# Optimization experiments

Measured on AMD Instinct MI355X. Metric: run time of the kernel, lower is better.

## Reference

```python
import jax, jax.numpy as jnp
import numpy as np

N_NODES = 50000
N_EDGES = 800000
IN_DIM = 128
HIDDEN = 128


def setup_inputs() -> dict:
    key = jax.random.key(0)
    ks = jax.random.split(key, 6)
    x = jax.random.normal(ks[0], (N_NODES, IN_DIM), dtype=jnp.float32)
    edge_index = jax.random.randint(ks[1], (2, N_EDGES), 0, N_NODES, dtype=jnp.int32)
    W1 = jax.random.normal(ks[2], (IN_DIM, HIDDEN), dtype=jnp.float32) * 0.05
    b1 = jnp.zeros((HIDDEN,), dtype=jnp.float32)
    W2 = jax.random.normal(ks[3], (HIDDEN, HIDDEN), dtype=jnp.float32) * 0.05
    b2 = jnp.zeros((HIDDEN,), dtype=jnp.float32)
    return {"x": x, "edge_index": edge_index, "W1": W1, "b1": b1, "W2": W2, "b2": b2}


def _gcn_conv(x, W, b, src, dst, norm, n):
    # PyG GCNConv: linear transform, then normalized sum-aggregate, then bias.
    h = x @ W                                  # [N, H]
    msg = h[src] * norm[:, None]               # gather + scale  [E+N, H]
    out = jax.ops.segment_sum(msg, dst, num_segments=n)
    return out + b


def reference(x, edge_index, W1, b1, W2, b2):
    n = x.shape[0]
    # add self-loops (GCNConv default add_self_loops=True)
    loops = jnp.arange(n, dtype=edge_index.dtype)
    src = jnp.concatenate([edge_index[0], loops])
    dst = jnp.concatenate([edge_index[1], loops])
    # symmetric normalization: deg over destination nodes (edge_weight = 1)
    deg = jax.ops.segment_sum(jnp.ones(src.shape, dtype=x.dtype), dst, num_segments=n)
    dinv = jax.lax.rsqrt(deg)                  # deg >= 1 because of self-loops
    norm = dinv[src] * dinv[dst]               # [E+N]
    h = jax.nn.relu(_gcn_conv(x, W1, b1, src, dst, norm, n))
    return _gcn_conv(h, W2, b2, src, dst, norm, n)
```

## Files before the change

### kernel.cpp

```cpp
#include <hip/hip_runtime.h>

#define N_NODES 50000
#define N_EDGES 800000
#define DIM 128
#define CHUNK 4096
#define GRID 196
#define SEG_CAP 6144
#define GEMM_BLOCKS 391
#define GA 196
#define GB (GEMM_BLOCKS - GA)

typedef __attribute__((ext_vector_type(8))) short bf16x8;
typedef __attribute__((ext_vector_type(4))) float f32x4;


__device__ inline unsigned rne_bf16(float f) {
    unsigned u = __float_as_uint(f);
    return (u + 0x7FFFu + ((u >> 16) & 1u)) >> 16;
}
__device__ inline unsigned pk_bf16(float a, float b) {
    return rne_bf16(a) | (rne_bf16(b) << 16);
}
__device__ inline float bf_lo(unsigned u) { return __uint_as_float(u << 16); }
__device__ inline float bf_hi(unsigned u) { return __uint_as_float(u & 0xFFFF0000u); }


__device__ void fragw_build(const float* __restrict__ W, uint4* __restrict__ fh,
                            uint4* __restrict__ fl, int slot) {
    const int lane = slot & 63, tile = slot >> 6;
    const int c = tile >> 2, q = tile & 3;
    const int k0 = q * 32 + ((lane >> 4) << 3);
    const int col = c * 16 + (lane & 15);
    unsigned h[8], l[8];
#pragma unroll
    for (int j = 0; j < 8; ++j) {
        float w = W[(size_t)(k0 + j) * DIM + col];
        unsigned hb = rne_bf16(w);
        h[j] = hb;
        l[j] = rne_bf16(w - __uint_as_float(hb << 16));
    }
    uint4 uh, ul;
    uh.x = h[0] | (h[1] << 16); uh.y = h[2] | (h[3] << 16);
    uh.z = h[4] | (h[5] << 16); uh.w = h[6] | (h[7] << 16);
    ul.x = l[0] | (l[1] << 16); ul.y = l[2] | (l[3] << 16);
    ul.z = l[4] | (l[5] << 16); ul.w = l[6] | (l[7] << 16);
    fh[slot] = uh;
    fl[slot] = ul;
}


__global__ __launch_bounds__(256) void chunk_hist_fragw(const int* __restrict__ dst,
                                                        int* __restrict__ chist,
                                                        const float* __restrict__ W1,
                                                        const float* __restrict__ W2,
                                                        uint4* f1h, uint4* f1l,
                                                        uint4* f2h, uint4* f2l) {
    const int bid = blockIdx.x;
    if (bid < GRID) {
        __shared__ int hist[256];
        const int t = threadIdx.x;
        const int eb = bid * CHUNK;
        const int cnt = min(CHUNK, N_EDGES - eb);
        hist[t] = 0;
        __syncthreads();
        for (int i = t; i < cnt; i += 256)
            atomicAdd(&hist[dst[eb + i] >> 8], 1);
        __syncthreads();
        chist[bid * 256 + t] = hist[t];
    } else {
        const int b2 = bid - GRID;
        const int slot = (b2 & 7) * 256 + threadIdx.x;
        if (b2 < 8) fragw_build(W1, f1h, f1l, slot);
        else        fragw_build(W2, f2h, f2l, slot);
    }
}


__device__ void gemm_body(const float* __restrict__ X,
                          const uint4* __restrict__ fWh,
                          const uint4* __restrict__ fWl,
                          uint2* __restrict__ O, int gb, char* smem) {
    const int t = threadIdx.x;

    {
        uint4* s4 = (uint4*)smem;
        for (int i = t; i < 2048; i += 256) {
            s4[i] = fWh[i];
            s4[2048 + i] = fWl[i];
        }
    }
    __syncthreads();

    const int w = t >> 6, lane = t & 63;
    const int lrow = lane & 15, lgrp = lane >> 4;
    const int rbase = gb * 128;

    bf16x8 Ah[2][4], Al[2][4];
#pragma unroll
    for (int m = 0; m < 2; ++m) {
        const int r = rbase + w * 32 + m * 16 + lrow;
        const bool ok = (r < N_NODES);
        const float4* xp = (const float4*)(X + (size_t)r * DIM + lgrp * 8);
#pragma unroll
        for (int q = 0; q < 4; ++q) {
            float4 a0 = ok ? xp[q * 8]     : make_float4(0.f, 0.f, 0.f, 0.f);
            float4 a1 = ok ? xp[q * 8 + 1] : make_float4(0.f, 0.f, 0.f, 0.f);
            float f[8] = {a0.x, a0.y, a0.z, a0.w, a1.x, a1.y, a1.z, a1.w};
            bf16x8 hi, lo;
#pragma unroll
            for (int j = 0; j < 8; ++j) {
                unsigned hb = rne_bf16(f[j]);
                hi[j] = (short)hb;
                lo[j] = (short)rne_bf16(f[j] - __uint_as_float(hb << 16));
            }
            Ah[m][q] = hi;
            Al[m][q] = lo;
        }
    }

    f32x4 acc[2][8];
#pragma unroll
    for (int m = 0; m < 2; ++m)
#pragma unroll
        for (int c = 0; c < 8; ++c)
            acc[m][c] = (f32x4){0.f, 0.f, 0.f, 0.f};

    const bf16x8* Bh = (const bf16x8*)smem;
    const bf16x8* Bl = (const bf16x8*)(smem + 32768);
#pragma unroll
    for (int c = 0; c < 8; ++c) {
#pragma unroll
        for (int q = 0; q < 4; ++q) {
            bf16x8 bh = Bh[(c * 4 + q) * 64 + lane];
            bf16x8 bl = Bl[(c * 4 + q) * 64 + lane];
#pragma unroll
            for (int m = 0; m < 2; ++m) {
                acc[m][c] = __builtin_amdgcn_mfma_f32_16x16x32_bf16(Ah[m][q], bh, acc[m][c], 0, 0, 0);
                acc[m][c] = __builtin_amdgcn_mfma_f32_16x16x32_bf16(Al[m][q], bh, acc[m][c], 0, 0, 0);
                acc[m][c] = __builtin_amdgcn_mfma_f32_16x16x32_bf16(Ah[m][q], bl, acc[m][c], 0, 0, 0);
            }
        }
    }

    __syncthreads();
    float* Lf = (float*)smem;
#pragma unroll
    for (int m = 0; m < 2; ++m)
#pragma unroll
        for (int c = 0; c < 8; ++c)
#pragma unroll
            for (int rg = 0; rg < 4; ++rg)
                Lf[(w * 32 + m * 16 + lgrp * 4 + rg) * DIM + c * 16 + lrow] = acc[m][c][rg];
    __syncthreads();

    const float4* Lf4 = (const float4*)smem;
    for (int idx = t; idx < 4096; idx += 256) {
        const int row = idx >> 5, s = idx & 31;
        const int gr = rbase + row;
        if (gr < N_NODES) {
            float4 v = Lf4[idx];
            uint2 o;
            o.x = pk_bf16(v.x, v.y);
            o.y = pk_bf16(v.z, v.w);
            O[(size_t)gr * 32 + s] = o;
        }
    }
}


__device__ void sort_scatter_body(const int* __restrict__ src,
                                  const int* __restrict__ dst,
                                  const int* __restrict__ chist,
                                  unsigned* __restrict__ sorted,
                                  int* __restrict__ bbase_g,
                                  int bid, char* smem) {
    int* hist  = (int*)smem;
    int* sc    = hist + 256;
    int* lbase = sc + 256;
    int* lcur  = lbase + 256;
    int* gbase = lcur + 256;
    unsigned* sl = (unsigned*)(smem + 5 * 1024);

    const int t = threadIdx.x;
    const int eb = bid * CHUNK;
    const int cnt = min(CHUNK, N_EDGES - eb);

    int sum = 0, myoff = 0;
    for (int c = 0; c < GRID; ++c) {
        int v = chist[c * 256 + t];
        if (c == bid) myoff = sum;
        sum += v;
    }
    hist[t] = chist[bid * 256 + t];
    sc[t] = sum;
    __syncthreads();
    for (int off = 1; off < 256; off <<= 1) {
        int u = (t >= off) ? sc[t - off] : 0;
        __syncthreads();
        sc[t] += u;
        __syncthreads();
    }
    gbase[t] = (sc[t] - sum) + myoff;
    if (bid == 0) bbase_g[t] = sc[t] - sum;
    __syncthreads();

    sc[t] = hist[t];
    __syncthreads();
    for (int off = 1; off < 256; off <<= 1) {
        int u = (t >= off) ? sc[t - off] : 0;
        __syncthreads();
        sc[t] += u;
        __syncthreads();
    }
    int ex = sc[t] - hist[t];
    lbase[t] = ex;
    lcur[t] = ex;
    __syncthreads();

    for (int i = t; i < cnt; i += 256) {
        int s = src[eb + i], d = dst[eb + i];
        int b = d >> 8;
        int p = atomicAdd(&lcur[b], 1);
        sl[p] = ((unsigned)b << 24) | ((unsigned)(d & 255) << 16) | (unsigned)s;
    }
    __syncthreads();
    for (int i = t; i < cnt; i += 256) {
        unsigned rec = sl[i];
        int b = rec >> 24;
        sorted[gbase[b] + (i - lbase[b])] = rec;
    }
}


__device__ void csr_build_body(const unsigned* __restrict__ sorted,
                               const int* __restrict__ bbase,
                               int* __restrict__ rowptr,
                               float* __restrict__ dinv,
                               int* __restrict__ csr,
                               int k, char* smem) {
    int* hist = (int*)smem;
    int* sc   = hist + 256;
    int* lcur = sc + 256;
    int* seg  = (int*)(smem + 3 * 1024);

    const int t = threadIdx.x;
    const int base = bbase[k];
    const int cntk = ((k == 255) ? N_EDGES : bbase[k + 1]) - base;
    if (k == 0 && t == 0) rowptr[N_NODES] = N_EDGES;

    hist[t] = 0;
    __syncthreads();
    for (int i = t; i < cntk; i += 256)
        atomicAdd(&hist[(sorted[base + i] >> 16) & 255], 1);
    __syncthreads();

    const int node = (k << 8) + t;
    const int dv = hist[t];
    if (node < N_NODES) dinv[node] = rsqrtf((float)dv + 1.0f);

    sc[t] = dv;
    __syncthreads();
    for (int off = 1; off < 256; off <<= 1) {
        int u = (t >= off) ? sc[t - off] : 0;
        __syncthreads();
        sc[t] += u;
        __syncthreads();
    }
    int ex = sc[t] - dv;
    if (node < N_NODES) rowptr[node] = base + ex;
    lcur[t] = ex;
    __syncthreads();

    if (cntk <= SEG_CAP) {
        for (int i = t; i < cntk; i += 256) {
            unsigned rec = sorted[base + i];
            int p = atomicAdd(&lcur[(rec >> 16) & 255], 1);
            seg[p] = (int)(rec & 0xFFFFu);
        }
        __syncthreads();
        for (int i = t; i < cntk; i += 256)
            csr[base + i] = seg[i];
    } else {
        for (int i = t; i < cntk; i += 256) {
            unsigned rec = sorted[base + i];
            int p = atomicAdd(&lcur[(rec >> 16) & 255], 1);
            csr[base + p] = (int)(rec & 0xFFFFu);
        }
    }
}


__global__ __launch_bounds__(256, 2) void sort_gemm(const int* __restrict__ src,
                                                    const int* __restrict__ dst,
                                                    const int* __restrict__ chist,
                                                    unsigned* __restrict__ sorted,
                                                    int* __restrict__ bbase_g,
                                                    const float* __restrict__ X,
                                                    const uint4* __restrict__ fWh,
                                                    const uint4* __restrict__ fWl,
                                                    uint2* __restrict__ O) {
    __shared__ __align__(16) char smem[65536];
    if (blockIdx.x < GRID)
        sort_scatter_body(src, dst, chist, sorted, bbase_g, blockIdx.x, smem);
    else
        gemm_body(X, fWh, fWl, O, blockIdx.x - GRID, smem);
}

__global__ __launch_bounds__(256, 2) void csr_gemm(const unsigned* __restrict__ sorted,
                                                   const int* __restrict__ bbase,
                                                   int* __restrict__ rowptr,
                                                   float* __restrict__ dinv,
                                                   int* __restrict__ csr,
                                                   const float* __restrict__ X,
                                                   const uint4* __restrict__ fWh,
                                                   const uint4* __restrict__ fWl,
                                                   uint2* __restrict__ O) {
    __shared__ __align__(16) char smem[65536];
    if (blockIdx.x < GRID)
        csr_build_body(sorted, bbase, rowptr, dinv, csr, blockIdx.x, smem);
    else
        gemm_body(X, fWh, fWl, O, blockIdx.x - GRID + GA, smem);
}


__device__ inline float4 agg_node(int node, const uint2* __restrict__ H2,
                                  const int* __restrict__ rowptr,
                                  const int* __restrict__ csr,
                                  const float* __restrict__ dinv,
                                  const float4* __restrict__ b4, int relu) {
    const int lane = threadIdx.x & 63;
    const int half = lane >> 5;
    const int col  = lane & 31;

    const float dn = dinv[node];
    float4 acc = make_float4(0.f, 0.f, 0.f, 0.f);
    if (half == 0) {
        uint2 v = H2[(size_t)node * 32 + col];
        acc.x = dn * bf_lo(v.x); acc.y = dn * bf_hi(v.x);
        acc.z = dn * bf_lo(v.y); acc.w = dn * bf_hi(v.y);
    }

    int j = rowptr[node];
    const int end = rowptr[node + 1];

#define ACC(v, ds) do { \
        acc.x = fmaf((ds), bf_lo((v).x), acc.x); \
        acc.y = fmaf((ds), bf_hi((v).x), acc.y); \
        acc.z = fmaf((ds), bf_lo((v).y), acc.z); \
        acc.w = fmaf((ds), bf_hi((v).y), acc.w); } while (0)

    for (; j + 16 <= end; j += 16) {
        int s0 = csr[j +  0 + half], s1 = csr[j +  2 + half];
        int s2 = csr[j +  4 + half], s3 = csr[j +  6 + half];
        int s4 = csr[j +  8 + half], s5 = csr[j + 10 + half];
        int s6 = csr[j + 12 + half], s7 = csr[j + 14 + half];
        uint2 v0 = H2[(size_t)s0 * 32 + col]; float d0 = dinv[s0];
        uint2 v1 = H2[(size_t)s1 * 32 + col]; float d1 = dinv[s1];
        uint2 v2 = H2[(size_t)s2 * 32 + col]; float d2 = dinv[s2];
        uint2 v3 = H2[(size_t)s3 * 32 + col]; float d3 = dinv[s3];
        uint2 v4 = H2[(size_t)s4 * 32 + col]; float d4 = dinv[s4];
        uint2 v5 = H2[(size_t)s5 * 32 + col]; float d5 = dinv[s5];
        uint2 v6 = H2[(size_t)s6 * 32 + col]; float d6 = dinv[s6];
        uint2 v7 = H2[(size_t)s7 * 32 + col]; float d7 = dinv[s7];
        ACC(v0, d0); ACC(v1, d1); ACC(v2, d2); ACC(v3, d3);
        ACC(v4, d4); ACC(v5, d5); ACC(v6, d6); ACC(v7, d7);
    }
    if (j + 8 <= end) {
        int s0 = csr[j + half], s1 = csr[j + 2 + half];
        int s2 = csr[j + 4 + half], s3 = csr[j + 6 + half];
        uint2 v0 = H2[(size_t)s0 * 32 + col]; float d0 = dinv[s0];
        uint2 v1 = H2[(size_t)s1 * 32 + col]; float d1 = dinv[s1];
        uint2 v2 = H2[(size_t)s2 * 32 + col]; float d2 = dinv[s2];
        uint2 v3 = H2[(size_t)s3 * 32 + col]; float d3 = dinv[s3];
        ACC(v0, d0); ACC(v1, d1); ACC(v2, d2); ACC(v3, d3);
        j += 8;
    }
    if (j + 4 <= end) {
        int s0 = csr[j + half], s1 = csr[j + 2 + half];
        uint2 v0 = H2[(size_t)s0 * 32 + col]; float d0 = dinv[s0];
        uint2 v1 = H2[(size_t)s1 * 32 + col]; float d1 = dinv[s1];
        ACC(v0, d0); ACC(v1, d1);
        j += 4;
    }
    if (j + 2 <= end) {
        int s = csr[j + half];
        uint2 v = H2[(size_t)s * 32 + col]; float d0 = dinv[s];
        ACC(v, d0);
        j += 2;
    }
    if (j < end && half == 0) {
        int s = csr[j];
        uint2 v = H2[(size_t)s * 32 + col]; float d0 = dinv[s];
        ACC(v, d0);
    }
#undef ACC

    acc.x += __shfl_xor(acc.x, 32, 64);
    acc.y += __shfl_xor(acc.y, 32, 64);
    acc.z += __shfl_xor(acc.z, 32, 64);
    acc.w += __shfl_xor(acc.w, 32, 64);

    float4 o = make_float4(0.f, 0.f, 0.f, 0.f);
    if (half == 0) {
        float4 bb = b4[col];
        o.x = acc.x * dn + bb.x;
        o.y = acc.y * dn + bb.y;
        o.z = acc.z * dn + bb.z;
        o.w = acc.w * dn + bb.w;
        if (relu) {
            o.x = fmaxf(o.x, 0.f); o.y = fmaxf(o.y, 0.f);
            o.z = fmaxf(o.z, 0.f); o.w = fmaxf(o.w, 0.f);
        }
    }
    return o;
}


__global__ __launch_bounds__(256) void aggregate_h1(const uint2* __restrict__ H2,
                                                    const int* __restrict__ rowptr,
                                                    const int* __restrict__ csr,
                                                    const float* __restrict__ dinv,
                                                    const float4* __restrict__ b4,
                                                    uint2* __restrict__ h1h,
                                                    uint2* __restrict__ h1l) {
    int node = blockIdx.x * 4 + (threadIdx.x >> 6);
    if (node >= N_NODES) return;
    float4 o = agg_node(node, H2, rowptr, csr, dinv, b4, 1);
    const int lane = threadIdx.x & 63;
    if (lane < 32) {
        unsigned hx = rne_bf16(o.x), hy = rne_bf16(o.y);
        unsigned hz = rne_bf16(o.z), hw = rne_bf16(o.w);
        unsigned lx = rne_bf16(o.x - __uint_as_float(hx << 16));
        unsigned ly = rne_bf16(o.y - __uint_as_float(hy << 16));
        unsigned lz = rne_bf16(o.z - __uint_as_float(hz << 16));
        unsigned lw = rne_bf16(o.w - __uint_as_float(hw << 16));
        uint2 hv; hv.x = hx | (hy << 16); hv.y = hz | (hw << 16);
        uint2 lv; lv.x = lx | (ly << 16); lv.y = lz | (lw << 16);
        h1h[(size_t)node * 32 + lane] = hv;
        h1l[(size_t)node * 32 + lane] = lv;
    }
}


__global__ __launch_bounds__(256) void aggregate_out(const uint2* __restrict__ H2,
                                                     const int* __restrict__ rowptr,
                                                     const int* __restrict__ csr,
                                                     const float* __restrict__ dinv,
                                                     const float4* __restrict__ b4,
                                                     float4* __restrict__ out) {
    int node = blockIdx.x * 4 + (threadIdx.x >> 6);
    if (node >= N_NODES) return;
    float4 o = agg_node(node, H2, rowptr, csr, dinv, b4, 0);
    const int lane = threadIdx.x & 63;
    if (lane < 32) out[(size_t)node * 32 + lane] = o;
}


__global__ __launch_bounds__(256, 2) void gemm_xw2(const uint2* __restrict__ h1h,
                                                   const uint2* __restrict__ h1l,
                                                   const uint4* __restrict__ fWh,
                                                   const uint4* __restrict__ fWl,
                                                   uint2* __restrict__ O) {
    __shared__ __align__(16) char smem[65536];
    const int t = threadIdx.x;

    {
        uint4* s4 = (uint4*)smem;
        for (int i = t; i < 2048; i += 256) {
            s4[i] = fWh[i];
            s4[2048 + i] = fWl[i];
        }
    }
    __syncthreads();

    const int w = t >> 6, lane = t & 63;
    const int lrow = lane & 15, lgrp = lane >> 4;
    const int rbase = blockIdx.x * 128;

    bf16x8 Ah[2][4], Al[2][4];
    const bf16x8 zz = (bf16x8){0,0,0,0,0,0,0,0};
#pragma unroll
    for (int m = 0; m < 2; ++m) {
        const int r = rbase + w * 32 + m * 16 + lrow;
        const bool ok = (r < N_NODES);
        const uint2* ph = h1h + (size_t)r * 32 + lgrp * 2;
        const uint2* pl = h1l + (size_t)r * 32 + lgrp * 2;
#pragma unroll
        for (int q = 0; q < 4; ++q) {
            Ah[m][q] = ok ? *(const bf16x8*)(ph + q * 8) : zz;
            Al[m][q] = ok ? *(const bf16x8*)(pl + q * 8) : zz;
        }
    }

    f32x4 acc[2][8];
#pragma unroll
    for (int m = 0; m < 2; ++m)
#pragma unroll
        for (int c = 0; c < 8; ++c)
            acc[m][c] = (f32x4){0.f, 0.f, 0.f, 0.f};

    const bf16x8* Bh = (const bf16x8*)smem;
    const bf16x8* Bl = (const bf16x8*)(smem + 32768);
#pragma unroll
    for (int c = 0; c < 8; ++c) {
#pragma unroll
        for (int q = 0; q < 4; ++q) {
            bf16x8 bh = Bh[(c * 4 + q) * 64 + lane];
            bf16x8 bl = Bl[(c * 4 + q) * 64 + lane];
#pragma unroll
            for (int m = 0; m < 2; ++m) {
                acc[m][c] = __builtin_amdgcn_mfma_f32_16x16x32_bf16(Ah[m][q], bh, acc[m][c], 0, 0, 0);
                acc[m][c] = __builtin_amdgcn_mfma_f32_16x16x32_bf16(Al[m][q], bh, acc[m][c], 0, 0, 0);
                acc[m][c] = __builtin_amdgcn_mfma_f32_16x16x32_bf16(Ah[m][q], bl, acc[m][c], 0, 0, 0);
            }
        }
    }

    __syncthreads();
    float* Lf = (float*)smem;
#pragma unroll
    for (int m = 0; m < 2; ++m)
#pragma unroll
        for (int c = 0; c < 8; ++c)
#pragma unroll
            for (int rg = 0; rg < 4; ++rg)
                Lf[(w * 32 + m * 16 + lgrp * 4 + rg) * DIM + c * 16 + lrow] = acc[m][c][rg];
    __syncthreads();

    const float4* Lf4 = (const float4*)smem;
    for (int idx = t; idx < 4096; idx += 256) {
        const int row = idx >> 5, s = idx & 31;
        const int gr = rbase + row;
        if (gr < N_NODES) {
            float4 v = Lf4[idx];
            uint2 o;
            o.x = pk_bf16(v.x, v.y);
            o.y = pk_bf16(v.z, v.w);
            O[(size_t)gr * 32 + s] = o;
        }
    }
}


extern "C" void kernel_launch(void* const* d_in, const int* in_sizes, int n_in,
                              void* d_out, int out_size, void* d_ws, size_t ws_size,
                              hipStream_t stream) {
    const float* x  = (const float*)d_in[0];
    const int*   ei = (const int*)d_in[1];
    const float* W1 = (const float*)d_in[2];
    const float* b1 = (const float*)d_in[3];
    const float* W2 = (const float*)d_in[4];
    const float* b2 = (const float*)d_in[5];
    float* out = (float*)d_out;

    const int* src = ei;
    const int* dst = ei + N_EDGES;

    char* p = (char*)d_ws;
    int*      chist  = (int*)p;              p += GRID * 256 * 4;
    float*    dinv   = (float*)p;            p += ((N_NODES * 4 + 1023) & ~1023);
    int*      rowptr = (int*)p;              p += (((N_NODES + 1) * 4 + 1023) & ~1023);
    unsigned* sorted = (unsigned*)p;         p += ((N_EDGES * 4 + 1023) & ~1023);
    int*      csr    = (int*)p;              p += ((N_EDGES * 4 + 1023) & ~1023);
    int*      bbase  = (int*)p;              p += 1024;
    uint4*    f1h    = (uint4*)p;            p += 32768;
    uint4*    f1l    = (uint4*)p;            p += 32768;
    uint4*    f2h    = (uint4*)p;            p += 32768;
    uint4*    f2l    = (uint4*)p;            p += 32768;
    uint2*    hp     = (uint2*)p;            p += (size_t)N_NODES * DIM * 2;
    uint2*    h1h    = (uint2*)p;            p += (size_t)N_NODES * DIM * 2;
    uint2*    h1l    = (uint2*)p;            p += (size_t)N_NODES * DIM * 2;
    uint2*    hp2    = (uint2*)p;

    const int aggBlocks = (N_NODES + 3) / 4;

    chunk_hist_fragw<<<GRID + 16, 256, 0, stream>>>(dst, chist, W1, W2,
                                                    f1h, f1l, f2h, f2l);
    sort_gemm<<<GRID + GA, 256, 0, stream>>>(src, dst, chist, sorted, bbase,
                                             x, f1h, f1l, hp);
    csr_gemm<<<GRID + GB, 256, 0, stream>>>(sorted, bbase, rowptr, dinv, csr,
                                            x, f1h, f1l, hp);

    aggregate_h1<<<aggBlocks, 256, 0, stream>>>(hp, rowptr, csr, dinv,
                                                (const float4*)b1, h1h, h1l);

    gemm_xw2<<<GEMM_BLOCKS, 256, 0, stream>>>(h1h, h1l, f2h, f2l, hp2);

    aggregate_out<<<aggBlocks, 256, 0, stream>>>(hp2, rowptr, csr, dinv,
                                                 (const float4*)b2, (float4*)out);
}
```

Before: 210.9 us.

## Prescale GEMM outputs by source dinv to drop per-edge dinv gathers

```diff
diff --git a/kernel.cpp b/kernel.cpp
--- a/kernel.cpp
+++ b/kernel.cpp
@@ -25,6 +25,12 @@
 __device__ inline float bf_hi(unsigned u) { return __uint_as_float(u & 0xFFFF0000u); }
 
 
+__global__ __launch_bounds__(256) void zero_deg(int* __restrict__ deg) {
+    const int i = blockIdx.x * 256 + threadIdx.x;
+    if (i < N_NODES) deg[i] = 0;
+}
+
+
 __device__ void fragw_build(const float* __restrict__ W, uint4* __restrict__ fh,
                             uint4* __restrict__ fl, int slot) {
     const int lane = slot & 63, tile = slot >> 6;
@@ -51,6 +57,7 @@
 
 __global__ __launch_bounds__(256) void chunk_hist_fragw(const int* __restrict__ dst,
                                                         int* __restrict__ chist,
+                                                        int* __restrict__ deg,
                                                         const float* __restrict__ W1,
                                                         const float* __restrict__ W2,
                                                         uint4* f1h, uint4* f1l,
@@ -63,8 +70,11 @@
         const int cnt = min(CHUNK, N_EDGES - eb);
         hist[t] = 0;
         __syncthreads();
-        for (int i = t; i < cnt; i += 256)
-            atomicAdd(&hist[dst[eb + i] >> 8], 1);
+        for (int i = t; i < cnt; i += 256) {
+            int d = dst[eb + i];
+            atomicAdd(&hist[d >> 8], 1);
+            atomicAdd(&deg[d], 1);
+        }
         __syncthreads();
         chist[bid * 256 + t] = hist[t];
     } else {
@@ -79,6 +89,7 @@
 __device__ void gemm_body(const float* __restrict__ X,
                           const uint4* __restrict__ fWh,
                           const uint4* __restrict__ fWl,
+                          const int* __restrict__ deg,
                           uint2* __restrict__ O, int gb, char* smem) {
     const int t = threadIdx.x;
 
@@ -158,10 +169,11 @@
         const int row = idx >> 5, s = idx & 31;
         const int gr = rbase + row;
         if (gr < N_NODES) {
+            float di = rsqrtf((float)deg[gr] + 1.0f);
             float4 v = Lf4[idx];
             uint2 o;
-            o.x = pk_bf16(v.x, v.y);
-            o.y = pk_bf16(v.z, v.w);
+            o.x = pk_bf16(v.x * di, v.y * di);
+            o.y = pk_bf16(v.z * di, v.w * di);
             O[(size_t)gr * 32 + s] = o;
         }
     }
@@ -298,12 +310,13 @@
                                                     const float* __restrict__ X,
                                                     const uint4* __restrict__ fWh,
                                                     const uint4* __restrict__ fWl,
+                                                    const int* __restrict__ deg,
                                                     uint2* __restrict__ O) {
     __shared__ __align__(16) char smem[65536];
     if (blockIdx.x < GRID)
         sort_scatter_body(src, dst, chist, sorted, bbase_g, blockIdx.x, smem);
     else
-        gemm_body(X, fWh, fWl, O, blockIdx.x - GRID, smem);
+        gemm_body(X, fWh, fWl, deg, O, blockIdx.x - GRID, smem);
 }
 
 __global__ __launch_bounds__(256, 2) void csr_gemm(const unsigned* __restrict__ sorted,
@@ -314,86 +327,84 @@
                                                    const float* __restrict__ X,
                                                    const uint4* __restrict__ fWh,
                                                    const uint4* __restrict__ fWl,
+                                                   const int* __restrict__ deg,
                                                    uint2* __restrict__ O) {
     __shared__ __align__(16) char smem[65536];
     if (blockIdx.x < GRID)
         csr_build_body(sorted, bbase, rowptr, dinv, csr, blockIdx.x, smem);
     else
-        gemm_body(X, fWh, fWl, O, blockIdx.x - GRID + GA, smem);
-}
-
-
-__device__ inline float4 agg_node(int node, const uint2* __restrict__ H2,
-                                  const int* __restrict__ rowptr,
-                                  const int* __restrict__ csr,
-                                  const float* __restrict__ dinv,
-                                  const float4* __restrict__ b4, int relu) {
+        gemm_body(X, fWh, fWl, deg, O, blockIdx.x - GRID + GA, smem);
+}
+
+
+__device__ inline float4 agg_node_ps(int node, const uint2* __restrict__ H2,
+                                     const int* __restrict__ rowptr,
+                                     const int* __restrict__ csr,
+                                     const float* __restrict__ dinv,
+                                     const float4* __restrict__ b4, int relu) {
     const int lane = threadIdx.x & 63;
     const int half = lane >> 5;
     const int col  = lane & 31;
 
-    const float dn = dinv[node];
     float4 acc = make_float4(0.f, 0.f, 0.f, 0.f);
     if (half == 0) {
         uint2 v = H2[(size_t)node * 32 + col];
-        acc.x = dn * bf_lo(v.x); acc.y = dn * bf_hi(v.x);
-        acc.z = dn * bf_lo(v.y); acc.w = dn * bf_hi(v.y);
+        acc.x = bf_lo(v.x); acc.y = bf_hi(v.x);
+        acc.z = bf_lo(v.y); acc.w = bf_hi(v.y);
     }
 
     int j = rowptr[node];
     const int end = rowptr[node + 1];
 
-#define ACC(v, ds) do { \
-        acc.x = fmaf((ds), bf_lo((v).x), acc.x); \
-        acc.y = fmaf((ds), bf_hi((v).x), acc.y); \
-        acc.z = fmaf((ds), bf_lo((v).y), acc.z); \
-        acc.w = fmaf((ds), bf_hi((v).y), acc.w); } while (0)
+#define ACCUM(v) do { \
+        acc.x += bf_lo((v).x); acc.y += bf_hi((v).x); \
+        acc.z += bf_lo((v).y); acc.w += bf_hi((v).y); } while (0)
 
     for (; j + 16 <= end; j += 16) {
         int s0 = csr[j +  0 + half], s1 = csr[j +  2 + half];
         int s2 = csr[j +  4 + half], s3 = csr[j +  6 + half];
         int s4 = csr[j +  8 + half], s5 = csr[j + 10 + half];
         int s6 = csr[j + 12 + half], s7 = csr[j + 14 + half];
-        uint2 v0 = H2[(size_t)s0 * 32 + col]; float d0 = dinv[s0];
-        uint2 v1 = H2[(size_t)s1 * 32 + col]; float d1 = dinv[s1];
-        uint2 v2 = H2[(size_t)s2 * 32 + col]; float d2 = dinv[s2];
-        uint2 v3 = H2[(size_t)s3 * 32 + col]; float d3 = dinv[s3];
-        uint2 v4 = H2[(size_t)s4 * 32 + col]; float d4 = dinv[s4];
-        uint2 v5 = H2[(size_t)s5 * 32 + col]; float d5 = dinv[s5];
-        uint2 v6 = H2[(size_t)s6 * 32 + col]; float d6 = dinv[s6];
-        uint2 v7 = H2[(size_t)s7 * 32 + col]; float d7 = dinv[s7];
-        ACC(v0, d0); ACC(v1, d1); ACC(v2, d2); ACC(v3, d3);
-        ACC(v4, d4); ACC(v5, d5); ACC(v6, d6); ACC(v7, d7);
+        uint2 v0 = H2[(size_t)s0 * 32 + col];
+        uint2 v1 = H2[(size_t)s1 * 32 + col];
+        uint2 v2 = H2[(size_t)s2 * 32 + col];
+        uint2 v3 = H2[(size_t)s3 * 32 + col];
+        uint2 v4 = H2[(size_t)s4 * 32 + col];
+        uint2 v5 = H2[(size_t)s5 * 32 + col];
+        uint2 v6 = H2[(size_t)s6 * 32 + col];
+        uint2 v7 = H2[(size_t)s7 * 32 + col];
+        ACCUM(v0); ACCUM(v1); ACCUM(v2); ACCUM(v3);
+        ACCUM(v4); ACCUM(v5); ACCUM(v6); ACCUM(v7);
     }
     if (j + 8 <= end) {
         int s0 = csr[j + half], s1 = csr[j + 2 + half];
         int s2 = csr[j + 4 + half], s3 = csr[j + 6 + half];
-        uint2 v0 = H2[(size_t)s0 * 32 + col]; float d0 = dinv[s0];
-        uint2 v1 = H2[(size_t)s1 * 32 + col]; float d1 = dinv[s1];
-        uint2 v2 = H2[(size_t)s2 * 32 + col]; float d2 = dinv[s2];
-        uint2 v3 = H2[(size_t)s3 * 32 + col]; float d3 = dinv[s3];
-        ACC(v0, d0); ACC(v1, d1); ACC(v2, d2); ACC(v3, d3);
+        uint2 v0 = H2[(size_t)s0 * 32 + col];
+        uint2 v1 = H2[(size_t)s1 * 32 + col];
+        uint2 v2 = H2[(size_t)s2 * 32 + col];
+        uint2 v3 = H2[(size_t)s3 * 32 + col];
+        ACCUM(v0); ACCUM(v1); ACCUM(v2); ACCUM(v3);
         j += 8;
     }
     if (j + 4 <= end) {
         int s0 = csr[j + half], s1 = csr[j + 2 + half];
-        uint2 v0 = H2[(size_t)s0 * 32 + col]; float d0 = dinv[s0];
-        uint2 v1 = H2[(size_t)s1 * 32 + col]; float d1 = dinv[s1];
-        ACC(v0, d0); ACC(v1, d1);
+        uint2 v0 = H2[(size_t)s0 * 32 + col];
+        uint2 v1 = H2[(size_t)s1 * 32 + col];
+        ACCUM(v0); ACCUM(v1);
         j += 4;
     }
     if (j + 2 <= end) {
         int s = csr[j + half];
-        uint2 v = H2[(size_t)s * 32 + col]; float d0 = dinv[s];
-        ACC(v, d0);
+        uint2 v = H2[(size_t)s * 32 + col];
+        ACCUM(v);
         j += 2;
     }
     if (j < end && half == 0) {
         int s = csr[j];
-        uint2 v = H2[(size_t)s * 32 + col]; float d0 = dinv[s];
-        ACC(v, d0);
-    }
-#undef ACC
+        uint2 v = H2[(size_t)s * 32 + col];
+        ACCUM(v);
+    }
+#undef ACCUM
 
     acc.x += __shfl_xor(acc.x, 32, 64);
     acc.y += __shfl_xor(acc.y, 32, 64);
@@ -402,6 +413,7 @@
 
     float4 o = make_float4(0.f, 0.f, 0.f, 0.f);
     if (half == 0) {
+        const float dn = dinv[node];
         float4 bb = b4[col];
         o.x = acc.x * dn + bb.x;
         o.y = acc.y * dn + bb.y;
@@ -425,9 +437,11 @@
                                                     uint2* __restrict__ h1l) {
     int node = blockIdx.x * 4 + (threadIdx.x >> 6);
     if (node >= N_NODES) return;
-    float4 o = agg_node(node, H2, rowptr, csr, dinv, b4, 1);
+    float4 o = agg_node_ps(node, H2, rowptr, csr, dinv, b4, 1);
     const int lane = threadIdx.x & 63;
     if (lane < 32) {
+        const float dn = dinv[node];
+        o.x *= dn; o.y *= dn; o.z *= dn; o.w *= dn;
         unsigned hx = rne_bf16(o.x), hy = rne_bf16(o.y);
         unsigned hz = rne_bf16(o.z), hw = rne_bf16(o.w);
         unsigned lx = rne_bf16(o.x - __uint_as_float(hx << 16));
@@ -450,7 +464,7 @@
                                                      float4* __restrict__ out) {
     int node = blockIdx.x * 4 + (threadIdx.x >> 6);
     if (node >= N_NODES) return;
-    float4 o = agg_node(node, H2, rowptr, csr, dinv, b4, 0);
+    float4 o = agg_node_ps(node, H2, rowptr, csr, dinv, b4, 0);
     const int lane = threadIdx.x & 63;
     if (lane < 32) out[(size_t)node * 32 + lane] = o;
 }
@@ -563,6 +577,7 @@
     unsigned* sorted = (unsigned*)p;         p += ((N_EDGES * 4 + 1023) & ~1023);
     int*      csr    = (int*)p;              p += ((N_EDGES * 4 + 1023) & ~1023);
     int*      bbase  = (int*)p;              p += 1024;
+    int*      deg    = (int*)p;              p += ((N_NODES * 4 + 1023) & ~1023);
     uint4*    f1h    = (uint4*)p;            p += 32768;
     uint4*    f1l    = (uint4*)p;            p += 32768;
     uint4*    f2h    = (uint4*)p;            p += 32768;
@@ -574,12 +589,13 @@
 
     const int aggBlocks = (N_NODES + 3) / 4;
 
-    chunk_hist_fragw<<<GRID + 16, 256, 0, stream>>>(dst, chist, W1, W2,
+    zero_deg<<<(N_NODES + 255) / 256, 256, 0, stream>>>(deg);
+    chunk_hist_fragw<<<GRID + 16, 256, 0, stream>>>(dst, chist, deg, W1, W2,
                                                     f1h, f1l, f2h, f2l);
     sort_gemm<<<GRID + GA, 256, 0, stream>>>(src, dst, chist, sorted, bbase,
-                                             x, f1h, f1l, hp);
+                                             x, f1h, f1l, deg, hp);
     csr_gemm<<<GRID + GB, 256, 0, stream>>>(sorted, bbase, rowptr, dinv, csr,
-                                            x, f1h, f1l, hp);
+                                            x, f1h, f1l, deg, hp);
 
     aggregate_h1<<<aggBlocks, 256, 0, stream>>>(hp, rowptr, csr, dinv,
                                                 (const float4*)b1, h1h, h1l);
```

Result: slower. 242.6 us (+15.0%).
